# Optimization experiments

Hardware: AMD Instinct MI355X
Metric: run time of the kernel (lower is better)

Reference implementation:

```python
import jax, jax.numpy as jnp
import numpy as np

NUM_GRAPHS = 10  # seq_len graphs batched together


def _gat_layer(x, W, al, ar, b, src, dst, n_nodes):
    # x: [N, h_dim]; W: [h_dim, H*D]; al/ar/b: [H, D]
    H, D = al.shape
    feat = (x @ W).reshape(-1, H, D)                      # [N, H, D]
    el = jnp.einsum('nhd,hd->nh', feat, al)               # [N, H]
    er = jnp.einsum('nhd,hd->nh', feat, ar)               # [N, H]
    e = jax.nn.leaky_relu(el[src] + er[dst], 0.2)         # [E, H]
    # edge softmax over incoming edges of each dst node (stable)
    emax = jax.ops.segment_max(e, dst, num_segments=n_nodes)
    emax = jnp.where(jnp.isfinite(emax), emax, 0.0)
    w = jnp.exp(e - emax[dst])                            # [E, H]
    denom = jax.ops.segment_sum(w, dst, num_segments=n_nodes)  # [N, H]
    msg = w[:, :, None] * feat[src]                       # [E, H, D]
    agg = jax.ops.segment_sum(msg, dst, num_segments=n_nodes)  # [N, H, D]
    out = agg / jnp.maximum(denom, 1e-9)[:, :, None] + b
    return out.mean(axis=1)                               # [N, h_dim] (mean over heads)


def setup_inputs() -> dict:
    key = jax.random.key(0)
    ks = jax.random.split(key, 16)
    N, E, V, h, H = 100000, 1000000, 50000, 64, 3
    node_ids = jax.random.randint(ks[0], (N,), 0, V)
    edge_src = jax.random.randint(ks[1], (E,), 0, N)
    edge_dst = jax.random.randint(ks[2], (E,), 0, N)
    node_graph_id = jnp.sort(jax.random.randint(ks[3], (N,), 0, NUM_GRAPHS))
    s = 1.0 / np.sqrt(h)
    return {
        'node_ids': node_ids, 'edge_src': edge_src, 'edge_dst': edge_dst,
        'node_graph_id': node_graph_id,
        'W_embed': jax.random.normal(ks[4], (V, h), jnp.float32),
        'W1': jax.random.normal(ks[5], (h, H * h), jnp.float32) * s,
        'al1': jax.random.normal(ks[6], (H, h), jnp.float32) * s,
        'ar1': jax.random.normal(ks[7], (H, h), jnp.float32) * s,
        'b1': jnp.zeros((H, h), jnp.float32),
        'W2': jax.random.normal(ks[8], (h, H * h), jnp.float32) * s,
        'al2': jax.random.normal(ks[9], (H, h), jnp.float32) * s,
        'ar2': jax.random.normal(ks[10], (H, h), jnp.float32) * s,
        'b2': jnp.zeros((H, h), jnp.float32),
    }


def reference(node_ids, edge_src, edge_dst, node_graph_id, W_embed,
              W1, al1, ar1, b1, W2, al2, ar2, b2):
    n_nodes = node_ids.shape[0]
    h = W_embed[node_ids]                                 # gather embeddings
    h = _gat_layer(h, W1, al1, ar1, b1, edge_src, edge_dst, n_nodes)
    h = _gat_layer(h, W2, al2, ar2, b2, edge_src, edge_dst, n_nodes)
    # dgl.max_nodes: per-graph max pooling over nodes
    global_info = jax.ops.segment_max(h, node_graph_id, num_segments=NUM_GRAPHS)
    return global_info                                    # [NUM_GRAPHS, h_dim]
```

## Files before the change

### kernel.cpp

```cpp
#include <hip/hip_runtime.h>
#include <math.h>


#define HEADS 3
#define HD 64
#define FDIM (HEADS*HD)
#define NCOL 208
#define NUM_GRAPHS 10
#define NPB 32
#define FROWB 384
#define PREPB 104
#define ECHUNK 1024

typedef short bf16x8 __attribute__((ext_vector_type(8)));
typedef float f32x4  __attribute__((ext_vector_type(4)));

__device__ __forceinline__ float bf2f(unsigned short u) {
    return __uint_as_float(((unsigned int)u) << 16);
}
__device__ __forceinline__ unsigned short f2bf(float f) {
    unsigned int u = __float_as_uint(f);
    unsigned int r = (u + 0x7FFFu + ((u >> 16) & 1u)) >> 16;
    return (unsigned short)r;
}

__device__ __forceinline__ int wave_incl_scan(int v, int lane) {
#pragma unroll
    for (int off = 1; off < 64; off <<= 1) {
        int t = __shfl_up(v, off);
        if (lane >= off) v += t;
    }
    return v;
}

__device__ __forceinline__ unsigned int fmap(float f) {
    unsigned int u = __float_as_uint(f);
    return (u & 0x80000000u) ? ~u : (u | 0x80000000u);
}
__device__ __forceinline__ float funmap(unsigned int u) {
    u = (u & 0x80000000u) ? (u & 0x7FFFFFFFu) : ~u;
    return __uint_as_float(u);
}

__global__ void k_prep_hist(const float* __restrict__ W1, const float* __restrict__ al1,
                            const float* __restrict__ ar1,
                            const float* __restrict__ W2, const float* __restrict__ al2,
                            const float* __restrict__ ar2,
                            unsigned short* __restrict__ Wt1, unsigned short* __restrict__ Wt2,
                            unsigned int* __restrict__ gm,
                            const int* __restrict__ dst, int* __restrict__ deg,
                            int* __restrict__ rank, int E) {
    if (blockIdx.x < PREPB) {
        int i = blockIdx.x * blockDim.x + threadIdx.x;
        if (i < 2 * NCOL * HD) {
            int l = i / (NCOL * HD), j = i % (NCOL * HD);
            int c = j >> 6, k = j & 63;
            const float* W  = l ? W2  : W1;
            const float* al = l ? al2 : al1;
            const float* ar = l ? ar2 : ar1;
            unsigned short* Wt = l ? Wt2 : Wt1;
            float v = 0.f;
            if (c < FDIM) {
                v = W[k * FDIM + c];
            } else if (c < FDIM + 6) {
                int h = c - FDIM;
                const float* a = (h < 3) ? al : ar;
                int hh = (h < 3) ? h : h - 3;
                float s = 0.f;
                for (int d = 0; d < HD; ++d)
                    s += W[k * FDIM + hh * HD + d] * a[hh * HD + d];
                v = s;
            }
            Wt[j] = f2bf(v);
        }
        if (i < NUM_GRAPHS * HD) gm[i] = 0x007FFFFFu;
    } else {
        int i = (blockIdx.x - PREPB) * blockDim.x + threadIdx.x;
        if (i < E) {
            int r = atomicAdd(&deg[dst[i]], 1);
            rank[i] = r;
        }
    }
}

__global__ void k_scan1(const int* __restrict__ deg, int* __restrict__ tmp,
                        int* __restrict__ partials, int N) {
    int t = threadIdx.x, b = blockIdx.x;
    int i = b * 256 + t;
    int v = (i < N) ? deg[i] : 0;
    int lane = t & 63, w = t >> 6;
    int incl = wave_incl_scan(v, lane);
    __shared__ int wsum[4];
    if (lane == 63) wsum[w] = incl;
    __syncthreads();
    int off = 0;
    for (int j = 0; j < w; ++j) off += wsum[j];
    incl += off;
    if (i < N) tmp[i] = incl;
    if (t == 255) partials[b] = incl;
}

__global__ void k_scan2(int* __restrict__ partials, int nb) {
    int t = threadIdx.x;
    int v = (t < nb) ? partials[t] : 0;
    int lane = t & 63, w = t >> 6;
    int incl = wave_incl_scan(v, lane);
    __shared__ int wsum[8];
    if (lane == 63) wsum[w] = incl;
    __syncthreads();
    int off = 0;
    for (int j = 0; j < w; ++j) off += wsum[j];
    incl += off;
    if (t < nb) partials[t] = incl;
}

__global__ void k_scan3(const int* __restrict__ tmp, const int* __restrict__ deg,
                        const int* __restrict__ partials, int* __restrict__ rowptr,
                        int N) {
    int i = blockIdx.x * blockDim.x + threadIdx.x;
    if (i >= N) return;
    int b = i >> 8;
    int off = b ? partials[b - 1] : 0;
    int incl = tmp[i] + off;
    rowptr[i + 1] = incl;
    if (i == 0) rowptr[0] = 0;
}

__device__ __forceinline__ void feat_body(
        const unsigned short* __restrict__ xbf, const int* __restrict__ ids,
        const float* __restrict__ Wemb, const unsigned short* __restrict__ Wt,
        unsigned char* __restrict__ featB, float4* __restrict__ el4,
        float4* __restrict__ er4, int N, int blk) {
    __shared__ unsigned short xs[NPB][72];
    __shared__ unsigned short ls[NPB][200];
    int t = threadIdx.x;
    int lane = t & 63, w = t >> 6;
    int base = blk * NPB;

    if (ids) {
        for (int i = t; i < NPB * 16; i += 256) {
            int row = i >> 4, c4 = (i & 15) * 4;
            int n = base + row;
            float4 v = {0.f, 0.f, 0.f, 0.f};
            if (n < N) v = *(const float4*)(Wemb + (size_t)ids[n] * HD + c4);
            unsigned short* dp = &xs[row][c4];
            dp[0] = f2bf(v.x); dp[1] = f2bf(v.y); dp[2] = f2bf(v.z); dp[3] = f2bf(v.w);
        }
    } else {
        for (int i = t; i < NPB * 16; i += 256) {
            int row = i >> 4, c4 = (i & 15) * 4;
            int n = base + row;
            ushort4 v = {0, 0, 0, 0};
            if (n < N) v = *(const ushort4*)(xbf + (size_t)n * HD + c4);
            *(ushort4*)(&xs[row][c4]) = v;
        }
    }

    int ntile = (w == 3) ? 4 : 3;
    bf16x8 bfrag[4][2];
#pragma unroll
    for (int c = 0; c < 4; ++c) {
        if (c >= ntile) break;
#pragma unroll
        for (int kk = 0; kk < 2; ++kk) {
            int coln = (w * 3 + c) * 16 + (lane & 15);
            int k0 = kk * 32 + (lane >> 4) * 8;
            bfrag[c][kk] = *(const bf16x8*)(Wt + (size_t)coln * HD + k0);
        }
    }
    __syncthreads();

    f32x4 acc[2][4];
#pragma unroll
    for (int r = 0; r < 2; ++r)
#pragma unroll
        for (int c = 0; c < 4; ++c) acc[r][c] = (f32x4){0.f, 0.f, 0.f, 0.f};
#pragma unroll
    for (int r = 0; r < 2; ++r)
#pragma unroll
        for (int kk = 0; kk < 2; ++kk) {
            int row = r * 16 + (lane & 15);
            int k0 = kk * 32 + (lane >> 4) * 8;
            bf16x8 a = *(const bf16x8*)(&xs[row][k0]);
#pragma unroll
            for (int c = 0; c < 4; ++c) {
                if (c >= ntile) break;
                acc[r][c] = __builtin_amdgcn_mfma_f32_16x16x32_bf16(a, bfrag[c][kk], acc[r][c], 0, 0, 0);
            }
        }

#pragma unroll
    for (int r = 0; r < 2; ++r)
#pragma unroll
        for (int c = 0; c < 3; ++c) {
            int col = (w * 3 + c) * 16 + (lane & 15);
#pragma unroll
            for (int j = 0; j < 4; ++j) {
                int row = r * 16 + (lane >> 4) * 4 + j;
                ls[row][col] = f2bf(acc[r][c][j]);
            }
        }

    if (w == 3) {
        int col = lane & 15;
        if (col < 6) {
#pragma unroll
            for (int r = 0; r < 2; ++r)
#pragma unroll
                for (int j = 0; j < 4; ++j) {
                    int row = r * 16 + (lane >> 4) * 4 + j;
                    int n = base + row;
                    if (n < N) {
                        float v = acc[r][3][j];
                        if (col < 3) ((float*)&el4[n])[col] = v;
                        else         ((float*)&er4[n])[col - 3] = v;
                    }
                }
        }
    }
    __syncthreads();

    for (int i = t; i < NPB * 64; i += 256) {
        int row = i >> 6, d = i & 63;
        int n = base + row;
        if (n < N) {
            unsigned int u = ((unsigned int)ls[row][64 + d] << 16) | (unsigned int)ls[row][d];
            *(unsigned int*)(featB + (size_t)n * FROWB + d * 4) = u;
        }
    }
    for (int i = t; i < NPB * 32; i += 256) {
        int row = i >> 5, dd = (i & 31) * 2;
        int n = base + row;
        if (n < N) {
            unsigned int u = (unsigned int)ls[row][128 + dd] |
                             ((unsigned int)ls[row][128 + dd + 1] << 16);
            *(unsigned int*)(featB + (size_t)n * FROWB + 256 + dd * 2) = u;
        }
    }
}

__global__ __launch_bounds__(256) void k_feat_mfma(
        const unsigned short* __restrict__ xbf, const int* __restrict__ ids,
        const float* __restrict__ Wemb, const unsigned short* __restrict__ Wt,
        unsigned char* __restrict__ featB, float4* __restrict__ el4,
        float4* __restrict__ er4, int N) {
    feat_body(xbf, ids, Wemb, Wt, featB, el4, er4, N, blockIdx.x);
}

__global__ __launch_bounds__(256) void k_feat1_scatter(
        const int* __restrict__ ids, const float* __restrict__ Wemb,
        const unsigned short* __restrict__ Wt,
        unsigned char* __restrict__ featB, float4* __restrict__ el4,
        float4* __restrict__ er4, int N,
        const int* __restrict__ src, const int* __restrict__ dst,
        const int* __restrict__ rank, const int* __restrict__ rowptr,
        int* __restrict__ csrc, int E, int NS8, int nsc8) {
    if ((int)blockIdx.x < nsc8) {
        int s = blockIdx.x;
        int lo = (s & 7) * NS8;
        int hi = lo + NS8;
        int i0 = (s >> 3) * ECHUNK + (int)threadIdx.x;
#pragma unroll
        for (int j = 0; j < ECHUNK / 256; ++j) {
            int i = i0 + j * 256;
            if (i < E) {
                int d = dst[i];
                if (d >= lo && d < hi) {
                    int pos = rowptr[d] + rank[i];
                    csrc[pos] = src[i];
                }
            }
        }
    } else {
        int fb = blockIdx.x - nsc8;
        if (fb * NPB < N)
            feat_body(nullptr, ids, Wemb, Wt, featB, el4, er4, N, fb);
    }
}

__global__ void k_gather(const int* __restrict__ rowptr, const int* __restrict__ csrc,
                         const float4* __restrict__ el4, const float4* __restrict__ er4,
                         const unsigned char* __restrict__ featB,
                         const float* __restrict__ b,
                         unsigned short* __restrict__ xout, int N) {
    __shared__ float4 stage[4][64];
    int wid = (blockIdx.x * blockDim.x + threadIdx.x) >> 6;
    int lane = threadIdx.x & 63, w = (threadIdx.x >> 6) & 3;
    if (wid >= N) return;
    int beg = rowptr[wid], end = rowptr[wid + 1];
    int deg = end - beg;
    float4 er = er4[wid];
    float acc0 = 0.f, acc1 = 0.f, acc2 = 0.f;
    float ds0 = 0.f, ds1 = 0.f, ds2 = 0.f;
    for (int cb = 0; cb < deg; cb += 64) {
        int nch = min(64, deg - cb);
        if (lane < nch) {
            int s = csrc[beg + cb + lane];
            float4 l = el4[s];
            float e0 = l.x + er.x; e0 = e0 >= 0.f ? e0 : 0.2f * e0;
            float e1 = l.y + er.y; e1 = e1 >= 0.f ? e1 : 0.2f * e1;
            float e2 = l.z + er.z; e2 = e2 >= 0.f ? e2 : 0.2f * e2;
            float4 o;
            o.x = __int_as_float(s);
            o.y = __expf(e0); o.z = __expf(e1); o.w = __expf(e2);
            stage[w][lane] = o;
        }
        __builtin_amdgcn_wave_barrier();
#pragma unroll 4
        for (int j = 0; j < nch; ++j) {
            float4 e = stage[w][j];
            int s = __float_as_int(e.x);
            const unsigned char* frow = featB + (size_t)s * FROWB;
            unsigned int u01 = *(const unsigned int*)(frow + (size_t)lane * 4);
            unsigned short h2 = *(const unsigned short*)(frow + 256 + (size_t)lane * 2);
            float f0 = __uint_as_float(u01 << 16);
            float f1 = __uint_as_float(u01 & 0xffff0000u);
            acc0 = fmaf(e.y, f0, acc0);
            acc1 = fmaf(e.z, f1, acc1);
            acc2 = fmaf(e.w, bf2f(h2), acc2);
            ds0 += e.y; ds1 += e.z; ds2 += e.w;
        }
        __builtin_amdgcn_wave_barrier();
    }
    float o = (acc0 / fmaxf(ds0, 1e-9f) + b[lane])
            + (acc1 / fmaxf(ds1, 1e-9f) + b[HD + lane])
            + (acc2 / fmaxf(ds2, 1e-9f) + b[2 * HD + lane]);
    xout[(size_t)wid * HD + lane] = f2bf(o * (1.f / 3.f));
}

__global__ void k_gmax(const unsigned short* __restrict__ x, const int* __restrict__ gid,
                       unsigned int* __restrict__ gm, int N) {
    int lane = threadIdx.x;
    int base = blockIdx.x * 64;
    int endn = min(base + 64, N);
    int cur = -1;
    float m = 0.f;
    for (int n = base; n < endn; ++n) {
        int g = gid[n];
        float v = bf2f(x[(size_t)n * HD + lane]);
        if (g != cur) {
            if (cur >= 0) atomicMax(&gm[cur * HD + lane], fmap(m));
            cur = g; m = v;
        } else {
            m = fmaxf(m, v);
        }
    }
    if (cur >= 0) atomicMax(&gm[cur * HD + lane], fmap(m));
}

__global__ void k_gmax_final(const unsigned int* __restrict__ gm, float* __restrict__ out) {
    int i = blockIdx.x * blockDim.x + threadIdx.x;
    if (i < NUM_GRAPHS * HD) out[i] = funmap(gm[i]);
}

extern "C" void kernel_launch(void* const* d_in, const int* in_sizes, int n_in,
                              void* d_out, int out_size, void* d_ws, size_t ws_size,
                              hipStream_t stream) {
    const int*   node_ids = (const int*)d_in[0];
    const int*   edge_src = (const int*)d_in[1];
    const int*   edge_dst = (const int*)d_in[2];
    const int*   gid      = (const int*)d_in[3];
    const float* Wemb     = (const float*)d_in[4];
    const float* W1  = (const float*)d_in[5];
    const float* al1 = (const float*)d_in[6];
    const float* ar1 = (const float*)d_in[7];
    const float* b1  = (const float*)d_in[8];
    const float* W2  = (const float*)d_in[9];
    const float* al2 = (const float*)d_in[10];
    const float* ar2 = (const float*)d_in[11];
    const float* b2  = (const float*)d_in[12];

    int N = in_sizes[0];
    int E = in_sizes[1];

    char* p = (char*)d_ws;
    auto alloc = [&](size_t bytes) {
        char* r = p;
        p += (bytes + 255) & ~(size_t)255;
        return (void*)r;
    };
    int*   deg      = (int*)alloc((size_t)N * 4);
    int*   tmp      = (int*)alloc((size_t)N * 4);
    int*   partials = (int*)alloc(512 * 4);
    int*   rowptr   = (int*)alloc((size_t)(N + 1) * 4);
    int*   rank     = (int*)alloc((size_t)E * 4);
    int*   csrc     = (int*)alloc((size_t)E * 4);
    unsigned char* featB = (unsigned char*)alloc((size_t)N * FROWB);
    unsigned short* Wt1  = (unsigned short*)alloc((size_t)NCOL * HD * 2);
    unsigned short* Wt2  = (unsigned short*)alloc((size_t)NCOL * HD * 2);
    float4* el4     = (float4*)alloc((size_t)N * 16);
    float4* er4     = (float4*)alloc((size_t)N * 16);
    unsigned short* x1b = (unsigned short*)alloc((size_t)N * HD * 2);
    unsigned int* gm = (unsigned int*)alloc(NUM_GRAPHS * HD * 4);
    (void)ws_size;

    int nb = (N + 255) / 256;

    hipMemsetAsync(deg, 0, (size_t)N * 4, stream);
    k_prep_hist<<<dim3(PREPB + (E + 255) / 256), dim3(256), 0, stream>>>(
        W1, al1, ar1, W2, al2, ar2, Wt1, Wt2, gm, edge_dst, deg, rank, E);
    k_scan1<<<dim3(nb), dim3(256), 0, stream>>>(deg, tmp, partials, N);
    k_scan2<<<dim3(1), dim3(512), 0, stream>>>(partials, nb);
    k_scan3<<<dim3(nb), dim3(256), 0, stream>>>(tmp, deg, partials, rowptr, N);

    dim3 featGrid((N + NPB - 1) / NPB), featBlk(256);
    dim3 aggGrid((N * 64 + 255) / 256), aggBlk(256);

    int nf = (N + NPB - 1) / NPB;
    int nchunks = (E + ECHUNK - 1) / ECHUNK;
    int nsc8 = nchunks * 8;
    int NS8 = (N + 7) / 8;
    dim3 fusedGrid(nsc8 + nf);

    k_feat1_scatter<<<fusedGrid, featBlk, 0, stream>>>(
        node_ids, Wemb, Wt1, featB, el4, er4, N,
        edge_src, edge_dst, rank, rowptr, csrc, E, NS8, nsc8);
    k_gather<<<aggGrid, aggBlk, 0, stream>>>(rowptr, csrc, el4, er4, featB, b1, x1b, N);

    k_feat_mfma<<<featGrid, featBlk, 0, stream>>>(x1b, nullptr, nullptr, Wt2,
                                                  featB, el4, er4, N);
    k_gather<<<aggGrid, aggBlk, 0, stream>>>(rowptr, csrc, el4, er4, featB, b2, x1b, N);

    k_gmax<<<dim3((N + 63) / 64), dim3(64), 0, stream>>>(x1b, gid, gm, N);
    k_gmax_final<<<dim3(1), dim3(NUM_GRAPHS * HD), 0, stream>>>(gm, (float*)d_out);
}
```

Baseline: 270.6 us.

## Co-schedule layer-1 feature MFMA with degree histogram instead of CSR scatter

The layer-1 feature transform was fused with the CSR scatter kernel. It now runs alongside the degree histogram atomics, and weight prep moves into a separate small kernel launched first. The histogram's atomic-heavy, latency-bound blocks can now overlap with the compute-bound feat blocks, and the scatter runs alone after the scan. The cost is one extra kernel launch, and feat1 now depends on a prep kernel that finishes just before it.

```diff
diff --git a/kernel.cpp b/kernel.cpp
--- a/kernel.cpp
+++ b/kernel.cpp
@@ -9,7 +9,6 @@
 #define NUM_GRAPHS 10
 #define NPB 32
 #define FROWB 384
-#define PREPB 104
 #define ECHUNK 1024
 
 typedef short bf16x8 __attribute__((ext_vector_type(8)));
@@ -42,45 +41,35 @@
     return __uint_as_float(u);
 }
 
-__global__ void k_prep_hist(const float* __restrict__ W1, const float* __restrict__ al1,
-                            const float* __restrict__ ar1,
-                            const float* __restrict__ W2, const float* __restrict__ al2,
-                            const float* __restrict__ ar2,
-                            unsigned short* __restrict__ Wt1, unsigned short* __restrict__ Wt2,
-                            unsigned int* __restrict__ gm,
-                            const int* __restrict__ dst, int* __restrict__ deg,
-                            int* __restrict__ rank, int E) {
-    if (blockIdx.x < PREPB) {
-        int i = blockIdx.x * blockDim.x + threadIdx.x;
-        if (i < 2 * NCOL * HD) {
-            int l = i / (NCOL * HD), j = i % (NCOL * HD);
-            int c = j >> 6, k = j & 63;
-            const float* W  = l ? W2  : W1;
-            const float* al = l ? al2 : al1;
-            const float* ar = l ? ar2 : ar1;
-            unsigned short* Wt = l ? Wt2 : Wt1;
-            float v = 0.f;
-            if (c < FDIM) {
-                v = W[k * FDIM + c];
-            } else if (c < FDIM + 6) {
-                int h = c - FDIM;
-                const float* a = (h < 3) ? al : ar;
-                int hh = (h < 3) ? h : h - 3;
-                float s = 0.f;
-                for (int d = 0; d < HD; ++d)
-                    s += W[k * FDIM + hh * HD + d] * a[hh * HD + d];
-                v = s;
-            }
-            Wt[j] = f2bf(v);
-        }
-        if (i < NUM_GRAPHS * HD) gm[i] = 0x007FFFFFu;
-    } else {
-        int i = (blockIdx.x - PREPB) * blockDim.x + threadIdx.x;
-        if (i < E) {
-            int r = atomicAdd(&deg[dst[i]], 1);
-            rank[i] = r;
-        }
-    }
+__global__ void k_prep(const float* __restrict__ W1, const float* __restrict__ al1,
+                       const float* __restrict__ ar1,
+                       const float* __restrict__ W2, const float* __restrict__ al2,
+                       const float* __restrict__ ar2,
+                       unsigned short* __restrict__ Wt1, unsigned short* __restrict__ Wt2,
+                       unsigned int* __restrict__ gm) {
+    int i = blockIdx.x * blockDim.x + threadIdx.x;
+    if (i < 2 * NCOL * HD) {
+        int l = i / (NCOL * HD), j = i % (NCOL * HD);
+        int c = j >> 6, k = j & 63;
+        const float* W  = l ? W2  : W1;
+        const float* al = l ? al2 : al1;
+        const float* ar = l ? ar2 : ar1;
+        unsigned short* Wt = l ? Wt2 : Wt1;
+        float v = 0.f;
+        if (c < FDIM) {
+            v = W[k * FDIM + c];
+        } else if (c < FDIM + 6) {
+            int h = c - FDIM;
+            const float* a = (h < 3) ? al : ar;
+            int hh = (h < 3) ? h : h - 3;
+            float s = 0.f;
+            for (int d = 0; d < HD; ++d)
+                s += W[k * FDIM + hh * HD + d] * a[hh * HD + d];
+            v = s;
+        }
+        Wt[j] = f2bf(v);
+    }
+    if (i < NUM_GRAPHS * HD) gm[i] = 0x007FFFFFu;
 }
 
 __global__ void k_scan1(const int* __restrict__ deg, int* __restrict__ tmp,
@@ -247,34 +236,44 @@
     feat_body(xbf, ids, Wemb, Wt, featB, el4, er4, N, blockIdx.x);
 }
 
-__global__ __launch_bounds__(256) void k_feat1_scatter(
+__global__ __launch_bounds__(256) void k_hist_feat1(
+        const int* __restrict__ dst, int* __restrict__ deg,
+        int* __restrict__ rank, int E, int nh,
         const int* __restrict__ ids, const float* __restrict__ Wemb,
         const unsigned short* __restrict__ Wt,
         unsigned char* __restrict__ featB, float4* __restrict__ el4,
-        float4* __restrict__ er4, int N,
+        float4* __restrict__ er4, int N) {
+    if ((int)blockIdx.x < nh) {
+        int i = blockIdx.x * 256 + (int)threadIdx.x;
+        if (i < E) {
+            int r = atomicAdd(&deg[dst[i]], 1);
+            rank[i] = r;
+        }
+    } else {
+        int fb = blockIdx.x - nh;
+        if (fb * NPB < N)
+            feat_body(nullptr, ids, Wemb, Wt, featB, el4, er4, N, fb);
+    }
+}
+
+__global__ __launch_bounds__(256) void k_scatter(
         const int* __restrict__ src, const int* __restrict__ dst,
         const int* __restrict__ rank, const int* __restrict__ rowptr,
-        int* __restrict__ csrc, int E, int NS8, int nsc8) {
-    if ((int)blockIdx.x < nsc8) {
-        int s = blockIdx.x;
-        int lo = (s & 7) * NS8;
-        int hi = lo + NS8;
-        int i0 = (s >> 3) * ECHUNK + (int)threadIdx.x;
-#pragma unroll
-        for (int j = 0; j < ECHUNK / 256; ++j) {
-            int i = i0 + j * 256;
-            if (i < E) {
-                int d = dst[i];
-                if (d >= lo && d < hi) {
-                    int pos = rowptr[d] + rank[i];
-                    csrc[pos] = src[i];
-                }
+        int* __restrict__ csrc, int E, int NS8) {
+    int s = blockIdx.x;
+    int lo = (s & 7) * NS8;
+    int hi = lo + NS8;
+    int i0 = (s >> 3) * ECHUNK + (int)threadIdx.x;
+#pragma unroll
+    for (int j = 0; j < ECHUNK / 256; ++j) {
+        int i = i0 + j * 256;
+        if (i < E) {
+            int d = dst[i];
+            if (d >= lo && d < hi) {
+                int pos = rowptr[d] + rank[i];
+                csrc[pos] = src[i];
             }
         }
-    } else {
-        int fb = blockIdx.x - nsc8;
-        if (fb * NPB < N)
-            feat_body(nullptr, ids, Wemb, Wt, featB, el4, er4, N, fb);
     }
 }
 
@@ -395,26 +394,29 @@
     (void)ws_size;
 
     int nb = (N + 255) / 256;
+    int nf = (N + NPB - 1) / NPB;
+    int nh = (E + 255) / 256;
 
     hipMemsetAsync(deg, 0, (size_t)N * 4, stream);
-    k_prep_hist<<<dim3(PREPB + (E + 255) / 256), dim3(256), 0, stream>>>(
-        W1, al1, ar1, W2, al2, ar2, Wt1, Wt2, gm, edge_dst, deg, rank, E);
+    k_prep<<<dim3((2 * NCOL * HD + 255) / 256), dim3(256), 0, stream>>>(
+        W1, al1, ar1, W2, al2, ar2, Wt1, Wt2, gm);
+
+    k_hist_feat1<<<dim3(nh + nf), dim3(256), 0, stream>>>(
+        edge_dst, deg, rank, E, nh,
+        node_ids, Wemb, Wt1, featB, el4, er4, N);
+
     k_scan1<<<dim3(nb), dim3(256), 0, stream>>>(deg, tmp, partials, N);
     k_scan2<<<dim3(1), dim3(512), 0, stream>>>(partials, nb);
     k_scan3<<<dim3(nb), dim3(256), 0, stream>>>(tmp, deg, partials, rowptr, N);
 
-    dim3 featGrid((N + NPB - 1) / NPB), featBlk(256);
+    int nchunks = (E + ECHUNK - 1) / ECHUNK;
+    int NS8 = (N + 7) / 8;
+    k_scatter<<<dim3(nchunks * 8), dim3(256), 0, stream>>>(
+        edge_src, edge_dst, rank, rowptr, csrc, E, NS8);
+
+    dim3 featGrid(nf), featBlk(256);
     dim3 aggGrid((N * 64 + 255) / 256), aggBlk(256);
 
-    int nf = (N + NPB - 1) / NPB;
-    int nchunks = (E + ECHUNK - 1) / ECHUNK;
-    int nsc8 = nchunks * 8;
-    int NS8 = (N + 7) / 8;
-    dim3 fusedGrid(nsc8 + nf);
-
-    k_feat1_scatter<<<fusedGrid, featBlk, 0, stream>>>(
-        node_ids, Wemb, Wt1, featB, el4, er4, N,
-        edge_src, edge_dst, rank, rowptr, csrc, E, NS8, nsc8);
     k_gather<<<aggGrid, aggBlk, 0, stream>>>(rowptr, csrc, el4, er4, featB, b1, x1b, N);
 
     k_feat_mfma<<<featGrid, featBlk, 0, stream>>>(x1b, nullptr, nullptr, Wt2,
```

New measurement: 273.7 us. About the same (+1.1%).
